# Optimization experiments

Hardware: AMD Instinct MI355X
Metric: run time of the kernel (lower is better)

## Reference

```python
import jax, jax.numpy as jnp
import numpy as np

N_, C_, H_, W_ = 8, 256, 64, 64
HEADS = 8
KS = 3
K2 = KS * KS
OUT = 256
HD = OUT // HEADS
STRIDE = 1
PAD = 1


def setup_inputs() -> dict:
    key = jax.random.key(0)
    ks = jax.random.split(key, 8)
    s = 0.05
    return {
        "input_features": jax.random.normal(ks[0], (N_, C_, H_, W_), jnp.float32),
        "Wq": jax.random.normal(ks[1], (OUT, C_), jnp.float32) * s,
        "Wk": jax.random.normal(ks[2], (OUT, C_), jnp.float32) * s,
        "Wv": jax.random.normal(ks[3], (OUT, C_), jnp.float32) * s,
        "off_w": jax.random.normal(ks[4], (HEADS * K2 * 2, C_, KS, KS), jnp.float32) * 0.01,
        "off_b": jnp.zeros((HEADS * K2 * 2,), jnp.float32),
        "attn_w": jax.random.normal(ks[5], (HEADS * K2, C_, KS, KS), jnp.float32) * 0.01,
        "attn_b": jnp.zeros((HEADS * K2,), jnp.float32),
        "Wo": jax.random.normal(ks[6], (OUT, OUT), jnp.float32) * s,
    }


def _conv2d(x, w, b):
    out = jax.lax.conv_general_dilated(
        x, w, (STRIDE, STRIDE), [(PAD, PAD), (PAD, PAD)],
        dimension_numbers=("NCHW", "OIHW", "NCHW"))
    return out + b[None, :, None, None]


def reference(input_features, Wq, Wk, Wv, off_w, off_b, attn_w, attn_b, Wo):
    x = input_features
    N, C, H, W = x.shape
    # query/key are projected but never used downstream in the original module
    q = jnp.einsum("oc,nchw->nohw", Wq, x)
    k = jnp.einsum("oc,nchw->nohw", Wk, x)
    v = jnp.einsum("oc,nchw->nohw", Wv, x)  # [N, OUT, H, W]

    offsets = _conv2d(x, off_w, off_b)                       # [N, HEADS*K2*2, Ho, Wo]
    aw = jax.nn.sigmoid(_conv2d(x, attn_w, attn_b))          # [N, HEADS*K2, Ho, Wo]
    Ho, Wo_sp = offsets.shape[2], offsets.shape[3]

    gx_base = jnp.linspace(-1.0, 1.0, Wo_sp)
    gy_base = jnp.linspace(-1.0, 1.0, Ho)

    # per-head, per-point (x,y) offsets, scaled by 2/[W,H] as in the source
    off = offsets.reshape(N, HEADS, K2, 2, Ho, Wo_sp)
    gx = gx_base[None, None, None, None, :] + off[:, :, :, 0] * (2.0 / W)  # [N,H,K2,Ho,Wo]
    gy = gy_base[None, None, None, :, None] + off[:, :, :, 1] * (2.0 / H)

    # grid_sample bilinear, align_corners=True, padding_mode='zeros'
    xp = (gx + 1.0) * 0.5 * (W - 1)
    yp = (gy + 1.0) * 0.5 * (H - 1)
    x0 = jnp.floor(xp).astype(jnp.int32)
    y0 = jnp.floor(yp).astype(jnp.int32)
    x1 = x0 + 1
    y1 = y0 + 1
    wx1 = xp - x0
    wx0 = 1.0 - wx1
    wy1 = yp - y0
    wy0 = 1.0 - wy1

    vf = v.reshape(N, HEADS, HD, H * W)

    def corner(yi, xi, wgt):
        valid = ((yi >= 0) & (yi < H) & (xi >= 0) & (xi < W)).astype(v.dtype)
        idx = (jnp.clip(yi, 0, H - 1) * W + jnp.clip(xi, 0, W - 1)).reshape(N, HEADS, -1)
        g = jnp.take_along_axis(vf, idx[:, :, None, :], axis=3)
        g = g.reshape(N, HEADS, HD, K2, Ho, Wo_sp)
        return g * (wgt * valid)[:, :, None]

    sampled = (corner(y0, x0, wy0 * wx0) + corner(y0, x1, wy0 * wx1)
               + corner(y1, x0, wy1 * wx0) + corner(y1, x1, wy1 * wx1))

    awr = aw.reshape(N, HEADS, K2, Ho, Wo_sp)
    head_out = jnp.einsum("nhckxy,nhkxy->nhcxy", sampled, awr)  # weighted sum over K2 points
    combined = head_out.reshape(N, OUT, Ho, Wo_sp)
    return jnp.einsum("oc,nchw->nohw", Wo, combined)
```

## Files before the change

kernel.cpp:

```cpp
#include <hip/hip_runtime.h>
#include <math.h>

#define N_    8
#define C_    256
#define H_    64
#define W_    64
#define HW    4096
#define OUT_  256
#define HEADS 8
#define HD    32
#define K2    9
#define OFFCH 144
#define AWCH  72
#define KTOT  2304
#define WPROWS 256
#define ABASE 16896

typedef __bf16 bf16x8 __attribute__((ext_vector_type(8)));
typedef __bf16 bf16x4 __attribute__((ext_vector_type(4)));
typedef float  f32x4  __attribute__((ext_vector_type(4)));

__device__ __forceinline__ void gload_lds16(const void* g, void* l) {
  __builtin_amdgcn_global_load_lds(
      (const __attribute__((address_space(1))) void*)g,
      (__attribute__((address_space(3))) void*)l, 16, 0, 0);
}

__global__ __launch_bounds__(256) void pack_x_kernel(
    const float* __restrict__ x, __bf16* __restrict__ xp)
{
  const int c0 = blockIdx.x << 6;
  const int y  = blockIdx.y;
  const int n  = blockIdx.z;
  const int tid = threadIdx.x;
  __shared__ float tile[64][65];

  const int tx = tid & 63, tg = tid >> 6;
#pragma unroll
  for (int i = 0; i < 16; ++i) {
    int cl = tg + (i << 2);
    tile[cl][tx] = x[((size_t)(n * C_ + c0 + cl) * H_ + y) * W_ + tx];
  }
  __syncthreads();
#pragma unroll
  for (int i = 0; i < 16; ++i) {
    int xl = tg + (i << 2);
    xp[((size_t)(n * HW) + y * W_ + xl) * C_ + c0 + tx] = (__bf16)tile[tx][xl];
  }
}

__global__ __launch_bounds__(256) void pack_w_kernel(
    const float* __restrict__ off_w, const float* __restrict__ off_b,
    const float* __restrict__ attn_w, const float* __restrict__ attn_b,
    __bf16* __restrict__ Wp, float* __restrict__ biasp,
    __bf16* __restrict__ zbuf)
{
  const int co = blockIdx.x;
  const int c  = threadIdx.x;
  if (co == 0) {
    *(uint4*)&zbuf[(size_t)c * 8] = make_uint4(0u, 0u, 0u, 0u);
  }
  const float* base = nullptr;
  if (co < OFFCH)      base = off_w  + ((size_t)co * C_ + c) * 9;
  else if (co < 216)   base = attn_w + ((size_t)(co - OFFCH) * C_ + c) * 9;
#pragma unroll
  for (int t = 0; t < 9; ++t) {
    float w = base ? base[t] : 0.f;
    Wp[(size_t)co * KTOT + t * C_ + c] = (__bf16)w;
  }
  if (c == 0) {
    float b = 0.f;
    if (co < OFFCH) b = off_b[co];
    else if (co < 216) b = attn_b[co - OFFCH];
    biasp[co] = b;
  }
}

__global__ __launch_bounds__(256) void pack_mat_kernel(
    const float* __restrict__ Wsrc, __bf16* __restrict__ Wdst)
{
  const int i = blockIdx.x * 256 + threadIdx.x;
  Wdst[i] = (__bf16)Wsrc[i];
}

__global__ __launch_bounds__(256) void conv_mfma_kernel(
    const __bf16* __restrict__ xp, const __bf16* __restrict__ Wp,
    const float* __restrict__ biasp, const __bf16* __restrict__ zbuf,
    __bf16* __restrict__ P2)
{
  const int yt = blockIdx.x;
  const int bn = blockIdx.y;
  const int n  = blockIdx.z;
  const int y0 = yt << 1;
  const int tid = threadIdx.x;
  const int lw = tid & 63, wv = tid >> 6;
  const int lr = lw & 15, lg = lw >> 4;

  __shared__ __align__(16) __bf16 smem[16896 + 12288];

  f32x4 acc[8][2];
#pragma unroll
  for (int m = 0; m < 8; ++m)
#pragma unroll
    for (int nt = 0; nt < 2; ++nt) acc[m][nt] = (f32x4){0.f, 0.f, 0.f, 0.f};

  if (tid < 64) {
    int p = tid & 3, cs = (tid >> 2) & 1, r = (tid >> 3) & 3, buf = tid >> 5;
    int col = cs ? 65 : 0;
    *(uint4*)&smem[((buf * 4 + r) * 66 + col) * 32 + p * 8] =
        make_uint4(0u, 0u, 0u, 0u);
  }

  int aoff[3][4];
#pragma unroll
  for (int d = 0; d < 3; ++d)
#pragma unroll
    for (int mm = 0; mm < 4; ++mm) {
      int col = (mm << 4) + lr + d;
      int p = lg ^ ((col >> 1) & 3);
      aoff[d][mm] = col * 32 + p * 8;
    }
  int boff[2];
#pragma unroll
  for (int nt = 0; nt < 2; ++nt) {
    int col = (nt << 4) + lr;
    int p = lg ^ ((col >> 1) & 3);
    boff[nt] = ABASE + wv * 3072 + col * 32 + p * 8;
  }

  const int scg = lw & 3;
  const __bf16* gB[2];
#pragma unroll
  for (int jj = 0; jj < 2; ++jj) {
    int col = (jj << 4) + (lw >> 2);
    int cg = scg ^ ((col >> 1) & 3);
    gB[jj] = Wp + (size_t)(bn * 128 + wv * 32 + col) * KTOT + (cg << 3);
  }
  const __bf16* gA[4];
  int aAdd;
  {
    int y = y0 - 1 + wv;
    bool valid = ((unsigned)y < (unsigned)H_);
    aAdd = valid ? 1 : 0;
#pragma unroll
    for (int k = 0; k < 4; ++k) {
      int col = 1 + (k << 4) + (lw >> 2);
      int cg = scg ^ ((col >> 1) & 3);
      gA[k] = valid
          ? xp + ((size_t)(n * HW) + y * W_ + (col - 1)) * C_ + (cg << 3)
          : zbuf;
    }
  }

  auto stageB = [&](int elemOff, int pbuf) {
#pragma unroll
    for (int jj = 0; jj < 2; ++jj)
      gload_lds16(gB[jj] + elemOff,
                  &smem[ABASE + wv * 3072 + pbuf * 1024 + (jj << 9)]);
  };
  auto stageA = [&](int c0elem, int buf) {
    const int add = aAdd ? c0elem : 0;
#pragma unroll
    for (int k = 0; k < 4; ++k)
      gload_lds16(gA[k] + add,
                  &smem[((buf * 4 + wv) * 66 + 1 + (k << 4)) * 32]);
  };

  stageA(0, 0);
  stageB(0 * C_ + 0, 0);
  stageB(1 * C_ + 0, 1);
  asm volatile("s_waitcnt vmcnt(4)" ::: "memory");
  __builtin_amdgcn_s_barrier();
  asm volatile("" ::: "memory");

  for (int cc = 0; cc < 4; ++cc) {
    const bool lastcc = (cc == 3);
#pragma unroll
    for (int sub = 0; sub < 2; ++sub) {
      const int ci = (cc << 1) + sub;
      const int abuf = sub;
#pragma unroll
      for (int tt = 0; tt < 9; ++tt) {
        const int dy = tt / 3, dxp = tt - dy * 3;
        const int pbR = tt % 3;
        const int pbW = (tt + 2) % 3;
        const bool lastSlice = lastcc && (sub == 1);

        if (tt == 1 && ci < 7) stageA((ci + 1) << 5, sub ^ 1);

        if (!(lastSlice && tt >= 7)) {
          const int tn  = (tt < 7) ? (tt + 2) : (tt - 7);
          const int cin = (tt < 7) ? ci : (ci + 1);
          stageB(tn * C_ + (cin << 5), pbW);
        }

        if (lastSlice && tt == 8)
          asm volatile("s_waitcnt vmcnt(0)" ::: "memory");
        else if (lastSlice && tt == 7)
          asm volatile("s_waitcnt vmcnt(2)" ::: "memory");
        else if ((tt == 1 || tt == 2) && ci < 7)
          asm volatile("s_waitcnt vmcnt(8)" ::: "memory");
        else
          asm volatile("s_waitcnt vmcnt(4)" ::: "memory");

        bf16x8 a[8], b[2];
#pragma unroll
        for (int m = 0; m < 8; ++m) {
          const int rr = (m >> 2) + dy;
          a[m] = *(const bf16x8*)&smem[aoff[dxp][m & 3] +
                                       (abuf * 4 + rr) * 2112];
        }
#pragma unroll
        for (int nt = 0; nt < 2; ++nt)
          b[nt] = *(const bf16x8*)&smem[boff[nt] + (pbR << 10)];

        __builtin_amdgcn_s_setprio(1);
#pragma unroll
        for (int m = 0; m < 8; ++m)
#pragma unroll
          for (int nt = 0; nt < 2; ++nt)
            acc[m][nt] = __builtin_amdgcn_mfma_f32_16x16x32_bf16(
                a[m], b[nt], acc[m][nt], 0, 0, 0);
        __builtin_amdgcn_s_setprio(0);

        if (tt == 8 && !lastSlice) {
          __builtin_amdgcn_s_barrier();
          asm volatile("" ::: "memory");
        }
      }
    }
  }

#pragma unroll
  for (int nt = 0; nt < 2; ++nt) {
    const int co = bn * 128 + wv * 32 + (nt << 4) + lr;
    if (co < 216) {
      const float bias = biasp[co];
      int idx;
      if (co < OFFCH) {
        int hh = co / 18;
        idx = (hh << 5) + (co - 18 * hh);
      } else {
        int r = co - OFFCH;
        int hh = r / 9;
        idx = (hh << 5) + 18 + (r - 9 * hh);
      }
#pragma unroll
      for (int m = 0; m < 8; ++m) {
#pragma unroll
        for (int reg = 0; reg < 4; ++reg) {
          const int sl = (m << 4) + (lg << 2) + reg;
          const int yout = y0 + (sl >> 6), xo = sl & 63;
          float v = acc[m][nt][reg] + bias;
          if (co >= OFFCH) v = 1.f / (1.f + expf(-v));
          P2[((size_t)n * HW + yout * W_ + xo) * 256 + idx] = (__bf16)v;
        }
      }
    }
  }
}

template <int MODE>
__global__ __launch_bounds__(256) void gemm256_kernel(
    const __bf16* __restrict__ A, const __bf16* __restrict__ Wb,
    __bf16* __restrict__ out_b, float* __restrict__ out_f)
{
  const int st = blockIdx.x;
  const int bn = blockIdx.y;
  const int n  = blockIdx.z;
  const int s0 = st << 7;
  const int tid = threadIdx.x;
  const int lw = tid & 63, wv = tid >> 6;
  const int lr = lw & 15, lg = lw >> 4;
  const int sm_base = wv << 5;

  __shared__ __align__(16) __bf16 smem[24576];

  f32x4 acc[2][8];
#pragma unroll
  for (int m = 0; m < 2; ++m)
#pragma unroll
    for (int nt = 0; nt < 8; ++nt) acc[m][nt] = (f32x4){0.f, 0.f, 0.f, 0.f};

  int aoff[2];
#pragma unroll
  for (int m = 0; m < 2; ++m) {
    int row = sm_base + (m << 4) + lr;
    int p = lg ^ ((row >> 1) & 3);
    aoff[m] = row * 32 + p * 8;
  }
  int boff[8];
#pragma unroll
  for (int nt = 0; nt < 8; ++nt) {
    int row = (nt << 4) + lr;
    int p = lg ^ ((row >> 1) & 3);
    boff[nt] = 12288 + row * 32 + p * 8;
  }

  const __bf16* gA[2];
  const __bf16* gB[2];
#pragma unroll
  for (int jj = 0; jj < 2; ++jj) {
    int j = wv * 2 + jj;
    int row = (j << 4) + (lw >> 2);
    int cg = (lw & 3) ^ ((row >> 1) & 3);
    gA[jj] = A + ((size_t)n * HW + s0 + row) * 256 + (cg << 3);
    gB[jj] = Wb + ((size_t)((bn << 7) + row)) * 256 + (cg << 3);
  }

  auto stage = [&](int k, int buf) {
    const int koff = k << 5;
#pragma unroll
    for (int jj = 0; jj < 2; ++jj)
      gload_lds16(gA[jj] + koff, &smem[buf * 4096 + ((wv * 2 + jj) << 9)]);
#pragma unroll
    for (int jj = 0; jj < 2; ++jj)
      gload_lds16(gB[jj] + koff,
                  &smem[12288 + buf * 4096 + ((wv * 2 + jj) << 9)]);
  };

  stage(0, 0);
  stage(1, 1);

#pragma unroll
  for (int k = 0; k < 8; ++k) {
    if (k < 7)
      asm volatile("s_waitcnt vmcnt(4)" ::: "memory");
    else
      asm volatile("s_waitcnt vmcnt(0)" ::: "memory");
    __builtin_amdgcn_s_barrier();
    asm volatile("" ::: "memory");

    if (k + 2 < 8) stage(k + 2, (k + 2) % 3);

    const int buf = k % 3;
    bf16x8 a[2], b[8];
#pragma unroll
    for (int m = 0; m < 2; ++m)
      a[m] = *(const bf16x8*)&smem[aoff[m] + buf * 4096];
#pragma unroll
    for (int nt = 0; nt < 8; ++nt)
      b[nt] = *(const bf16x8*)&smem[boff[nt] + buf * 4096];

    __builtin_amdgcn_s_setprio(1);
#pragma unroll
    for (int m = 0; m < 2; ++m)
#pragma unroll
      for (int nt = 0; nt < 8; ++nt)
        acc[m][nt] = __builtin_amdgcn_mfma_f32_16x16x32_bf16(
            a[m], b[nt], acc[m][nt], 0, 0, 0);
    __builtin_amdgcn_s_setprio(0);
  }

#pragma unroll
  for (int m = 0; m < 2; ++m) {
#pragma unroll
    for (int nt = 0; nt < 8; ++nt) {
      const int co = (bn << 7) + (nt << 4) + lr;
      if (MODE == 0) {
#pragma unroll
        for (int reg = 0; reg < 4; ++reg) {
          const int sm = sm_base + (m << 4) + (lg << 2) + reg;
          out_b[((size_t)n * HW + s0 + sm) * 256 + co] = (__bf16)acc[m][nt][reg];
        }
      } else {
        const int sm = sm_base + (m << 4) + (lg << 2);
        float4 v4 = make_float4(acc[m][nt][0], acc[m][nt][1],
                                acc[m][nt][2], acc[m][nt][3]);
        *(float4*)&out_f[((size_t)(n * 256 + co)) * HW + s0 + sm] = v4;
      }
    }
  }
}

__global__ __launch_bounds__(256) void sample_kernel(
    const __bf16* __restrict__ vtb, const __bf16* __restrict__ P2,
    __bf16* __restrict__ comb)
{
  const int b = blockIdx.x;
  const int y = b & 63;
  const int h = (b >> 6) & 7;
  const int n = b >> 9;
  const int tid = threadIdx.x;
  const int xq = tid >> 2, cg = tid & 3;
  const int lw = tid & 63, wv = tid >> 6;

  __shared__ __align__(16) __bf16 vsl[8 * 64 * 32];

  const int xs = (wv << 4) + (lw >> 2);
  const int cs = lw & 3;
  const __bf16* vrow0 =
      vtb + ((size_t)n * HW) * 256 + (h << 5) + (cs << 3) + (size_t)xs * 256;
#pragma unroll
  for (int r = 0; r < 8; ++r) {
    int yy = y - 3 + r;
    if ((unsigned)yy < (unsigned)H_)
      gload_lds16(vrow0 + (size_t)yy * (64 * 256),
                  &vsl[(r * 64 + (wv << 4)) * 32]);
  }

  const __bf16* prow = P2 + ((size_t)n * HW + y * 64 + xq) * 256 + (h << 5);
  bf16x8 p0 = *(const bf16x8*)(prow);
  bf16x8 p1 = *(const bf16x8*)(prow + 8);
  bf16x8 p2 = *(const bf16x8*)(prow + 16);
  bf16x4 p3 = *(const bf16x4*)(prow + 24);

  __syncthreads();

  float acc[8];
#pragma unroll
  for (int j = 0; j < 8; ++j) acc[j] = 0.f;

  const __bf16* vbase = vtb + ((size_t)n * HW) * 256 + (h << 5) + (cg << 3);

#pragma unroll
  for (int k = 0; k < K2; ++k) {
    float offx, offy, a;
    if (k < 4)      { offx = (float)p0[2 * k];       offy = (float)p0[2 * k + 1]; }
    else if (k < 8) { offx = (float)p1[2 * (k - 4)]; offy = (float)p1[2 * (k - 4) + 1]; }
    else            { offx = (float)p2[0];           offy = (float)p2[1]; }
    if (k < 6)      a = (float)p2[2 + k];
    else            a = (float)p3[k - 6];

    const float xpf = (float)xq + offx * (63.f / 64.f);
    const float ypf = (float)y  + offy * (63.f / 64.f);
    const float fx0 = floorf(xpf), fy0 = floorf(ypf);
    const int x0 = (int)fx0, y0 = (int)fy0;
    const float wx1 = xpf - fx0, wx0 = 1.f - wx1;
    const float wy1 = ypf - fy0, wy0 = 1.f - wy1;

#pragma unroll
    for (int cy = 0; cy < 2; ++cy) {
      const int yi = y0 + cy;
      if ((unsigned)yi >= (unsigned)H_) continue;
      const float wy = cy ? wy1 : wy0;
      const int ridx = yi - (y - 3);
#pragma unroll
      for (int cx = 0; cx < 2; ++cx) {
        const int xi = x0 + cx;
        if ((unsigned)xi >= (unsigned)W_) continue;
        const float cw = a * wy * (cx ? wx1 : wx0);
        bf16x8 v;
        if ((unsigned)ridx < 8u) {
          v = *(const bf16x8*)&vsl[(ridx * 64 + xi) * 32 + (cg << 3)];
        } else {
          v = *(const bf16x8*)(vbase + (size_t)(yi * W_ + xi) * 256);
        }
#pragma unroll
        for (int j = 0; j < 8; ++j) acc[j] = fmaf(cw, (float)v[j], acc[j]);
      }
    }
  }

  bf16x8 r;
#pragma unroll
  for (int j = 0; j < 8; ++j) r[j] = (__bf16)acc[j];
  *(bf16x8*)&comb[((size_t)n * HW + y * 64 + xq) * 256 + (h << 5) + (cg << 3)] = r;
}

extern "C" void kernel_launch(void* const* d_in, const int* in_sizes, int n_in,
                              void* d_out, int out_size, void* d_ws,
                              size_t ws_size, hipStream_t stream)
{
  const float* x      = (const float*)d_in[0];
  const float* Wv     = (const float*)d_in[3];
  const float* off_w  = (const float*)d_in[4];
  const float* off_b  = (const float*)d_in[5];
  const float* attn_w = (const float*)d_in[6];
  const float* attn_b = (const float*)d_in[7];
  const float* Wo     = (const float*)d_in[8];
  float* out = (float*)d_out;

  __bf16* vtb   = (__bf16*)d_ws;
  __bf16* xp    = vtb + (size_t)N_ * HW * OUT_;
  __bf16* comb  = xp + (size_t)N_ * HW * C_;
  __bf16* P2    = comb + (size_t)N_ * HW * OUT_;
  __bf16* Wp    = P2 + (size_t)N_ * HW * 256;
  __bf16* Wvb   = Wp + (size_t)WPROWS * KTOT;
  __bf16* Wob   = Wvb + (size_t)OUT_ * C_;
  __bf16* zbuf  = Wob + (size_t)OUT_ * OUT_;
  float*  biasp = (float*)(zbuf + 2048);

  pack_w_kernel<<<dim3(256), 256, 0, stream>>>(off_w, off_b, attn_w, attn_b,
                                               Wp, biasp, zbuf);
  pack_mat_kernel<<<dim3(256), 256, 0, stream>>>(Wv, Wvb);
  pack_mat_kernel<<<dim3(256), 256, 0, stream>>>(Wo, Wob);
  pack_x_kernel<<<dim3(4, 64, N_), 256, 0, stream>>>(x, xp);
  conv_mfma_kernel<<<dim3(32, 2, N_), 256, 0, stream>>>(xp, Wp, biasp, zbuf, P2);
  gemm256_kernel<0><<<dim3(32, 2, N_), 256, 0, stream>>>(xp, Wvb, vtb, nullptr);
  sample_kernel<<<dim3(N_ * HEADS * H_), 256, 0, stream>>>(vtb, P2, comb);
  gemm256_kernel<1><<<dim3(32, 2, N_), 256, 0, stream>>>(comb, Wob, nullptr,
                                                         out);
}
```

Measured before the change: 117.6 us.

## Retile conv MFMA warps into 2x2 grid with double-buffered weight slices

```diff
diff --git a/kernel.cpp b/kernel.cpp
--- a/kernel.cpp
+++ b/kernel.cpp
@@ -95,14 +95,15 @@
   const int tid = threadIdx.x;
   const int lw = tid & 63, wv = tid >> 6;
   const int lr = lw & 15, lg = lw >> 4;
-
-  __shared__ __align__(16) __bf16 smem[16896 + 12288];
-
-  f32x4 acc[8][2];
-#pragma unroll
-  for (int m = 0; m < 8; ++m)
-#pragma unroll
-    for (int nt = 0; nt < 2; ++nt) acc[m][nt] = (f32x4){0.f, 0.f, 0.f, 0.f};
+  const int wvM = wv >> 1, wvN = wv & 1;
+
+  __shared__ __align__(16) __bf16 smem[16896 + 16384];
+
+  f32x4 acc[4][4];
+#pragma unroll
+  for (int m = 0; m < 4; ++m)
+#pragma unroll
+    for (int nt = 0; nt < 4; ++nt) acc[m][nt] = (f32x4){0.f, 0.f, 0.f, 0.f};
 
   if (tid < 64) {
     int p = tid & 3, cs = (tid >> 2) & 1, r = (tid >> 3) & 3, buf = tid >> 5;
@@ -120,21 +121,21 @@
       int p = lg ^ ((col >> 1) & 3);
       aoff[d][mm] = col * 32 + p * 8;
     }
-  int boff[2];
-#pragma unroll
-  for (int nt = 0; nt < 2; ++nt) {
-    int col = (nt << 4) + lr;
-    int p = lg ^ ((col >> 1) & 3);
-    boff[nt] = ABASE + wv * 3072 + col * 32 + p * 8;
+  int boff[4];
+#pragma unroll
+  for (int nt = 0; nt < 4; ++nt) {
+    int row = (nt << 4) + lr;
+    int p = lg ^ ((row >> 1) & 3);
+    boff[nt] = ABASE + wv * 4096 + row * 32 + p * 8;
   }
 
   const int scg = lw & 3;
-  const __bf16* gB[2];
-#pragma unroll
-  for (int jj = 0; jj < 2; ++jj) {
-    int col = (jj << 4) + (lw >> 2);
-    int cg = scg ^ ((col >> 1) & 3);
-    gB[jj] = Wp + (size_t)(bn * 128 + wv * 32 + col) * KTOT + (cg << 3);
+  const __bf16* gB[4];
+#pragma unroll
+  for (int j = 0; j < 4; ++j) {
+    int row = (j << 4) + (lw >> 2);
+    int cg = scg ^ ((row >> 1) & 3);
+    gB[j] = Wp + (size_t)(bn * 128 + wvN * 64 + row) * KTOT + (cg << 3);
   }
   const __bf16* gA[4];
   int aAdd;
@@ -152,11 +153,11 @@
     }
   }
 
-  auto stageB = [&](int elemOff, int pbuf) {
-#pragma unroll
-    for (int jj = 0; jj < 2; ++jj)
-      gload_lds16(gB[jj] + elemOff,
-                  &smem[ABASE + wv * 3072 + pbuf * 1024 + (jj << 9)]);
+  auto stageB = [&](int elemOff, int pb) {
+#pragma unroll
+    for (int j = 0; j < 4; ++j)
+      gload_lds16(gB[j] + elemOff,
+                  &smem[ABASE + wv * 4096 + pb * 2048 + (j << 9)]);
   };
   auto stageA = [&](int c0elem, int buf) {
     const int add = aAdd ? c0elem : 0;
@@ -167,8 +168,7 @@
   };
 
   stageA(0, 0);
-  stageB(0 * C_ + 0, 0);
-  stageB(1 * C_ + 0, 1);
+  stageB(0, 0);
   asm volatile("s_waitcnt vmcnt(4)" ::: "memory");
   __builtin_amdgcn_s_barrier();
   asm volatile("" ::: "memory");
@@ -182,43 +182,39 @@
 #pragma unroll
       for (int tt = 0; tt < 9; ++tt) {
         const int dy = tt / 3, dxp = tt - dy * 3;
-        const int pbR = tt % 3;
-        const int pbW = (tt + 2) % 3;
+        const int pbR = (sub + tt) & 1;
+        const int pbW = (sub + tt + 1) & 1;
         const bool lastSlice = lastcc && (sub == 1);
 
         if (tt == 1 && ci < 7) stageA((ci + 1) << 5, sub ^ 1);
 
-        if (!(lastSlice && tt >= 7)) {
-          const int tn  = (tt < 7) ? (tt + 2) : (tt - 7);
-          const int cin = (tt < 7) ? ci : (ci + 1);
+        if (!(lastSlice && tt == 8)) {
+          const int tn  = (tt < 8) ? (tt + 1) : 0;
+          const int cin = (tt < 8) ? ci : (ci + 1);
           stageB(tn * C_ + (cin << 5), pbW);
         }
 
         if (lastSlice && tt == 8)
           asm volatile("s_waitcnt vmcnt(0)" ::: "memory");
-        else if (lastSlice && tt == 7)
-          asm volatile("s_waitcnt vmcnt(2)" ::: "memory");
-        else if ((tt == 1 || tt == 2) && ci < 7)
+        else if (tt == 1 && ci < 7)
           asm volatile("s_waitcnt vmcnt(8)" ::: "memory");
         else
           asm volatile("s_waitcnt vmcnt(4)" ::: "memory");
 
-        bf16x8 a[8], b[2];
-#pragma unroll
-        for (int m = 0; m < 8; ++m) {
-          const int rr = (m >> 2) + dy;
-          a[m] = *(const bf16x8*)&smem[aoff[dxp][m & 3] +
-                                       (abuf * 4 + rr) * 2112];
-        }
-#pragma unroll
-        for (int nt = 0; nt < 2; ++nt)
-          b[nt] = *(const bf16x8*)&smem[boff[nt] + (pbR << 10)];
+        const int rr = wvM + dy;
+        bf16x8 a[4], b[4];
+#pragma unroll
+        for (int m = 0; m < 4; ++m)
+          a[m] = *(const bf16x8*)&smem[aoff[dxp][m] + (abuf * 4 + rr) * 2112];
+#pragma unroll
+        for (int nt = 0; nt < 4; ++nt)
+          b[nt] = *(const bf16x8*)&smem[boff[nt] + (pbR << 11)];
 
         __builtin_amdgcn_s_setprio(1);
 #pragma unroll
-        for (int m = 0; m < 8; ++m)
-#pragma unroll
-          for (int nt = 0; nt < 2; ++nt)
+        for (int m = 0; m < 4; ++m)
+#pragma unroll
+          for (int nt = 0; nt < 4; ++nt)
             acc[m][nt] = __builtin_amdgcn_mfma_f32_16x16x32_bf16(
                 a[m], b[nt], acc[m][nt], 0, 0, 0);
         __builtin_amdgcn_s_setprio(0);
@@ -231,9 +227,10 @@
     }
   }
 
-#pragma unroll
-  for (int nt = 0; nt < 2; ++nt) {
-    const int co = bn * 128 + wv * 32 + (nt << 4) + lr;
+  const int yout = y0 + wvM;
+#pragma unroll
+  for (int nt = 0; nt < 4; ++nt) {
+    const int co = bn * 128 + wvN * 64 + (nt << 4) + lr;
     if (co < 216) {
       const float bias = biasp[co];
       int idx;
@@ -246,11 +243,10 @@
         idx = (hh << 5) + 18 + (r - 9 * hh);
       }
 #pragma unroll
-      for (int m = 0; m < 8; ++m) {
+      for (int m = 0; m < 4; ++m) {
 #pragma unroll
         for (int reg = 0; reg < 4; ++reg) {
-          const int sl = (m << 4) + (lg << 2) + reg;
-          const int yout = y0 + (sl >> 6), xo = sl & 63;
+          const int xo = (m << 4) + (lg << 2) + reg;
           float v = acc[m][nt][reg] + bias;
           if (co >= OFFCH) v = 1.f / (1.f + expf(-v));
           P2[((size_t)n * HW + yout * W_ + xo) * 256 + idx] = (__bf16)v;
```

Measured after the change: 120.1 us. 1.02x slower.
